# Optimization experiments

Hardware: AMD Instinct MI355X
Metric: run time of the kernel (lower is better)

The kernel has to match this reference:

```python
import jax, jax.numpy as jnp
import numpy as np

B, N_PER_G, H, K, A, GNN_STEPS = 64, 100, 64, 5, 50, 3
N = B * N_PER_G  # total nodes


def _lin(key, din, dout):
    s = 1.0 / np.sqrt(din)
    kw, kb = jax.random.split(key)
    w = jax.random.uniform(kw, (din, dout), minval=-s, maxval=s, dtype=jnp.float32)
    b = jax.random.uniform(kb, (dout,), minval=-s, maxval=s, dtype=jnp.float32)
    return w, b


def setup_inputs() -> dict:
    key = jax.random.key(0)
    ks = jax.random.split(key, 16)
    # complete graph (no self loops) per batch graph
    i, j = np.meshgrid(np.arange(N_PER_G), np.arange(N_PER_G), indexing="ij")
    m = i != j
    s0, d0 = i[m], j[m]  # [n*(n-1)]
    offs = (np.arange(B) * N_PER_G)[:, None]
    src = jnp.asarray((s0[None, :] + offs).reshape(-1), dtype=jnp.int32)
    dst = jnp.asarray((d0[None, :] + offs).reshape(-1), dtype=jnp.int32)
    E = src.shape[0]
    e_type = jax.random.uniform(ks[0], (E, 2), dtype=jnp.float32)
    d = jax.random.uniform(ks[1], (E, 1), dtype=jnp.float32)
    label = jax.nn.one_hot(jax.random.randint(ks[2], (N,), 0, K), K, dtype=jnp.float32)
    actions = jax.random.randint(ks[3], (B * A, 2), 0, N_PER_G)
    l1_w, l1_b = _lin(ks[4], K, H)
    l2_w, l2_b = _lin(ks[5], H, H)
    t3_w, t3_b = _lin(ks[6], H, H)
    t4_wf, t4_b = _lin(ks[7], 1, H)
    t5_wf, t5_b = _lin(ks[8], H, 1)
    t6_w, t6_b = _lin(ks[9], H, H)
    t7_1_w, t7_1_b = _lin(ks[10], H, H)
    t7_2_w, t7_2_b = _lin(ks[11], H, H)
    t9_1_w, t9_1_b = _lin(ks[12], H, H)
    t9_2_w, t9_2_b = _lin(ks[13], H, H)
    return dict(label=label, e_type=e_type, d=d,
                l1_w=l1_w, l1_b=l1_b, l2_w=l2_w, l2_b=l2_b,
                t3_w=t3_w, t3_b=t3_b, t4_w=t4_wf[0], t4_b=t4_b,
                t5_w=t5_wf[:, 0], t5_b=t5_b, t6_w=t6_w, t6_b=t6_b,
                t7_1_w=t7_1_w, t7_1_b=t7_1_b, t7_2_w=t7_2_w, t7_2_b=t7_2_b,
                t9_1_w=t9_1_w, t9_1_b=t9_1_b, t9_2_w=t9_2_w, t9_2_b=t9_2_b,
                src=src, dst=dst, actions=actions)


def reference(label, e_type, d, l1_w, l1_b, l2_w, l2_b, t3_w, t3_b, t4_w, t4_b,
              t5_w, t5_b, t6_w, t6_b, t7_1_w, t7_1_b, t7_2_w, t7_2_b,
              t9_1_w, t9_1_b, t9_2_w, t9_2_b, src, dst, actions):
    e1 = e_type[:, 0]
    # n1_hd = h[src]*e1, n1_d = d*e1; bmm(n1_hd^T, n1_d) == sum over in-edges of h[src]*e1^2*d
    w_e = (e1 * e1) * d[:, 0]                              # [E]
    s_e = d[:, 0] * e1                                     # per-edge n1_d scalar [E]
    # sum_deg relu(t4(n1_d)) as edge-parallel relu + scatter-add
    t4_edge = jax.nn.relu(s_e[:, None] * t4_w[None, :] + t4_b)   # [E,H]
    t4_sum = jax.ops.segment_sum(t4_edge, dst, num_segments=N)   # [N,H]
    base = label @ l1_w + l1_b + t4_sum @ t3_w + t3_b            # constant across gnn steps
    h = jnp.zeros((N, H), dtype=label.dtype)
    for _ in range(GNN_STEPS):
        n1_h = jax.ops.segment_sum(h[src] * w_e[:, None], dst, num_segments=N)  # [N,H]
        h = jax.nn.relu(base + n1_h @ l2_w + l2_b)
    # readout (forward_): graph mean -> t6 stem; per-action node-pair branch
    stem = h.reshape(B, N_PER_G, H).mean(axis=1) @ t6_w + t6_b    # [B,H]
    h2 = h @ t7_1_w + t7_1_b                                      # [N,H]
    offs = jnp.repeat(jnp.arange(B, dtype=actions.dtype) * N_PER_G, A)
    a = actions + offs[:, None]                                   # global node ids [B*A,2]
    ha = h2[a[:, 0]] + h2[a[:, 1]]                                # [B*A,H]
    u = jax.nn.relu(jax.nn.relu(ha) @ t7_2_w + t7_2_b) @ t9_2_w + t9_2_b
    g_branch = jax.nn.relu(stem) @ t9_1_w + t9_1_b                # [B,H]
    q = jax.nn.relu(g_branch[:, None, :] + u.reshape(B, A, H))    # [B,A,H]
    Q_sa = q.reshape(B * A, H) @ t5_w + t5_b[0]                   # [B*A]
    return Q_sa
```

## Files before the change

### kernel.cpp

```cpp
#include <hip/hip_runtime.h>

#define HD 64
#define NPG 100
#define NGRP 64
#define NACT 50
#define EPG 9900

typedef const float* fcp;

__global__ __launch_bounds__(1024)
void k_fused(fcp label, fcp e_type, fcp dvec,
             fcp l1_w, fcp l1_b, fcp l2_w, fcp l2_b,
             fcp t3_w, fcp t3_b, fcp t4_w, fcp t4_b,
             fcp t5_w, fcp t5_b, fcp t6_w, fcp t6_b,
             fcp t7_1_w, fcp t7_1_b, fcp t7_2_w, fcp t7_2_b,
             fcp t9_1_w, fcp t9_1_b, fcp t9_2_w, fcp t9_2_b,
             const int* __restrict__ actions,
             float* __restrict__ out)
{
    const int g  = blockIdx.x;
    const int t  = threadIdx.x;
    const int hh = t & 63;
    const int w  = t >> 6;

    __shared__ __align__(16) float sh_h[NPG * HD];
    __shared__ __align__(16) float sh_wt[NPG * NPG];
    __shared__ __align__(16) float sh_s[NPG * NPG];
    __shared__ __align__(16) float awk[16 * HD];
    __shared__ float gbuf[HD];

    float l1r[5];
    #pragma unroll
    for (int kk = 0; kk < 5; ++kk) l1r[kk] = l1_w[kk * HD + hh];

    float basev[7];
    #pragma unroll
    for (int m = 0; m < 7; ++m) {
        const int j = w + 16 * m;
        float x = 0.f;
        if (j < NPG) {
            #pragma unroll
            for (int kk = 0; kk < 5; ++kk)
                x += label[(g * NPG + j) * 5 + kk] * l1r[kk];
        }
        basev[m] = x;
    }

    int a0r[4], a1r[4];
    #pragma unroll
    for (int m = 0; m < 4; ++m) {
        const int al = w + 15 * m;
        a0r[m] = 0; a1r[m] = 0;
        if (w < 15 && al < NACT) {
            const int a = g * NACT + al;
            a0r[m] = actions[a * 2 + 0];
            a1r[m] = actions[a * 2 + 1];
        }
    }

    const int ebase = g * EPG;
    for (int idx = t; idx < NPG * NPG; idx += 1024) {
        const int i = idx / NPG;
        const int j = idx - i * NPG;
        float s = 0.f, wv = 0.f;
        if (i != j) {
            const int e = ebase + i * 99 + j - (j > i ? 1 : 0);
            const float e1 = e_type[2 * e];
            const float dd = dvec[e];
            s  = dd * e1;
            wv = e1 * e1 * dd;
        }
        sh_s[j * NPG + i]  = s;
        sh_wt[j * NPG + i] = wv;
    }
    __syncthreads();

    const float w4  = t4_w[hh];
    const float b4  = t4_b[hh];
    const float rb4 = fmaxf(b4, 0.f);
    #pragma unroll
    for (int m = 0; m < 7; ++m) {
        const int j = w + 16 * m;
        if (j < NPG) {
            float a0 = 0.f, a1 = 0.f, a2 = 0.f, a3 = 0.f;
            #pragma unroll 5
            for (int ib = 0; ib < 25; ++ib) {
                const float4 s4 = *(const float4*)&sh_s[j * NPG + 4 * ib];
                a0 += fmaxf(s4.x * w4 + b4, 0.f);
                a1 += fmaxf(s4.y * w4 + b4, 0.f);
                a2 += fmaxf(s4.z * w4 + b4, 0.f);
                a3 += fmaxf(s4.w * w4 + b4, 0.f);
            }
            sh_h[j * HD + hh] = (a0 + a1) + (a2 + a3) - rb4;
        }
    }

    const float bb   = l1_b[hh] + t3_b[hh];
    const float l2bv = l2_b[hh];
    #pragma unroll
    for (int m = 0; m < 7; ++m) basev[m] += bb;
    for (int ib = 0; ib < 16; ++ib) {
        const float tw0 = t3_w[(4 * ib + 0) * HD + hh];
        const float tw1 = t3_w[(4 * ib + 1) * HD + hh];
        const float tw2 = t3_w[(4 * ib + 2) * HD + hh];
        const float tw3 = t3_w[(4 * ib + 3) * HD + hh];
        #pragma unroll
        for (int m = 0; m < 7; ++m) {
            const int j = w + 16 * m;
            if (j < NPG) {
                const float4 x4 = *(const float4*)&sh_h[j * HD + 4 * ib];
                basev[m] += x4.x * tw0 + x4.y * tw1 + x4.z * tw2 + x4.w * tw3;
            }
        }
    }
    #pragma unroll
    for (int m = 0; m < 7; ++m) {
        const int j = w + 16 * m;
        if (j < NPG) sh_h[j * HD + hh] = fmaxf(basev[m] + l2bv, 0.f);
    }
    __syncthreads();

    #pragma unroll 1
    for (int step = 0; step < 2; ++step) {
        float acc[7];
        #pragma unroll
        for (int m = 0; m < 7; ++m) acc[m] = 0.f;
        for (int ib = 0; ib < 25; ++ib) {
            const float h0 = sh_h[(4 * ib + 0) * HD + hh];
            const float h1 = sh_h[(4 * ib + 1) * HD + hh];
            const float h2 = sh_h[(4 * ib + 2) * HD + hh];
            const float h3 = sh_h[(4 * ib + 3) * HD + hh];
            #pragma unroll
            for (int m = 0; m < 7; ++m) {
                const int j = w + 16 * m;
                if (j < NPG) {
                    const float4 wv = *(const float4*)&sh_wt[j * NPG + 4 * ib];
                    acc[m] += wv.x * h0 + wv.y * h1 + wv.z * h2 + wv.w * h3;
                }
            }
        }
        #pragma unroll
        for (int m = 0; m < 7; ++m) {
            const int j = w + 16 * m;
            if (j < NPG) sh_s[j * HD + hh] = acc[m];
        }
        float v[7];
        #pragma unroll
        for (int m = 0; m < 7; ++m) v[m] = basev[m] + l2bv;
        for (int ib = 0; ib < 16; ++ib) {
            const float w0 = l2_w[(4 * ib + 0) * HD + hh];
            const float w1 = l2_w[(4 * ib + 1) * HD + hh];
            const float w2 = l2_w[(4 * ib + 2) * HD + hh];
            const float w3 = l2_w[(4 * ib + 3) * HD + hh];
            #pragma unroll
            for (int m = 0; m < 7; ++m) {
                const int j = w + 16 * m;
                if (j < NPG) {
                    const float4 x4 = *(const float4*)&sh_s[j * HD + 4 * ib];
                    v[m] += x4.x * w0 + x4.y * w1 + x4.z * w2 + x4.w * w3;
                }
            }
        }
        __syncthreads();
        #pragma unroll
        for (int m = 0; m < 7; ++m) {
            const int j = w + 16 * m;
            if (j < NPG) sh_h[j * HD + hh] = fmaxf(v[m], 0.f);
        }
        __syncthreads();
    }

    {
        float ml = 0.f;
        for (int j = w; j < NPG; j += 16) ml += sh_h[j * HD + hh];
        awk[w * HD + hh] = ml;
    }
    float* hsum = sh_s;
    float* r1s  = sh_s + NACT * HD;
    if (w < 15) {
        #pragma unroll
        for (int m = 0; m < 4; ++m) {
            const int al = w + 15 * m;
            if (al < NACT)
                hsum[al * HD + hh] = sh_h[a0r[m] * HD + hh] + sh_h[a1r[m] * HD + hh];
        }
    }
    __syncthreads();

    if (w == 15) {
        float ml = 0.f;
        #pragma unroll
        for (int ww = 0; ww < 16; ++ww) ml += awk[ww * HD + hh];
        ml *= (1.f / NPG);
        float s = t6_b[hh];
        #pragma unroll 8
        for (int q = 0; q < HD; ++q) s += __shfl(ml, q, 64) * t6_w[q * HD + hh];
        s = fmaxf(s, 0.f);
        float gb = t9_1_b[hh];
        #pragma unroll 8
        for (int q = 0; q < HD; ++q) gb += __shfl(s, q, 64) * t9_1_w[q * HD + hh];
        gbuf[hh] = gb;
    } else {
        const float b71 = 2.f * t7_1_b[hh];
        float r[4];
        #pragma unroll
        for (int m = 0; m < 4; ++m) r[m] = b71;
        for (int ib = 0; ib < 16; ++ib) {
            const float w0 = t7_1_w[(4 * ib + 0) * HD + hh];
            const float w1 = t7_1_w[(4 * ib + 1) * HD + hh];
            const float w2 = t7_1_w[(4 * ib + 2) * HD + hh];
            const float w3 = t7_1_w[(4 * ib + 3) * HD + hh];
            #pragma unroll
            for (int m = 0; m < 4; ++m) {
                const int al = w + 15 * m;
                if (al < NACT) {
                    const float4 x4 = *(const float4*)&hsum[al * HD + 4 * ib];
                    r[m] += x4.x * w0 + x4.y * w1 + x4.z * w2 + x4.w * w3;
                }
            }
        }
        #pragma unroll
        for (int m = 0; m < 4; ++m) {
            const int al = w + 15 * m;
            if (al < NACT) r1s[al * HD + hh] = fmaxf(r[m], 0.f);
        }
        const float b72 = t7_2_b[hh];
        #pragma unroll
        for (int m = 0; m < 4; ++m) r[m] = b72;
        for (int ib = 0; ib < 16; ++ib) {
            const float w0 = t7_2_w[(4 * ib + 0) * HD + hh];
            const float w1 = t7_2_w[(4 * ib + 1) * HD + hh];
            const float w2 = t7_2_w[(4 * ib + 2) * HD + hh];
            const float w3 = t7_2_w[(4 * ib + 3) * HD + hh];
            #pragma unroll
            for (int m = 0; m < 4; ++m) {
                const int al = w + 15 * m;
                if (al < NACT) {
                    const float4 x4 = *(const float4*)&r1s[al * HD + 4 * ib];
                    r[m] += x4.x * w0 + x4.y * w1 + x4.z * w2 + x4.w * w3;
                }
            }
        }
        #pragma unroll
        for (int m = 0; m < 4; ++m) {
            const int al = w + 15 * m;
            if (al < NACT) hsum[al * HD + hh] = fmaxf(r[m], 0.f);
        }
    }
    __syncthreads();

    if (w < 15) {
        const float b92  = t9_2_b[hh];
        const float t5wv = t5_w[hh];
        const float t5bv = t5_b[0];
        const float gbv  = gbuf[hh];
        float u[4];
        #pragma unroll
        for (int m = 0; m < 4; ++m) u[m] = b92;
        for (int ib = 0; ib < 16; ++ib) {
            const float w0 = t9_2_w[(4 * ib + 0) * HD + hh];
            const float w1 = t9_2_w[(4 * ib + 1) * HD + hh];
            const float w2 = t9_2_w[(4 * ib + 2) * HD + hh];
            const float w3 = t9_2_w[(4 * ib + 3) * HD + hh];
            #pragma unroll
            for (int m = 0; m < 4; ++m) {
                const int al = w + 15 * m;
                if (al < NACT) {
                    const float4 x4 = *(const float4*)&hsum[al * HD + 4 * ib];
                    u[m] += x4.x * w0 + x4.y * w1 + x4.z * w2 + x4.w * w3;
                }
            }
        }
        #pragma unroll
        for (int m = 0; m < 4; ++m) {
            const int al = w + 15 * m;
            float qv = fmaxf(gbv + u[m], 0.f) * t5wv;
            #pragma unroll
            for (int off = 32; off > 0; off >>= 1) qv += __shfl_xor(qv, off, 64);
            if (al < NACT && hh == 0) out[g * NACT + al] = qv + t5bv;
        }
    }
}

extern "C" void kernel_launch(void* const* d_in, const int* in_sizes, int n_in,
                              void* d_out, int out_size, void* d_ws, size_t ws_size,
                              hipStream_t stream)
{
    fcp label  = (fcp)d_in[0];
    fcp e_type = (fcp)d_in[1];
    fcp dvec   = (fcp)d_in[2];
    fcp l1_w   = (fcp)d_in[3];
    fcp l1_b   = (fcp)d_in[4];
    fcp l2_w   = (fcp)d_in[5];
    fcp l2_b   = (fcp)d_in[6];
    fcp t3_w   = (fcp)d_in[7];
    fcp t3_b   = (fcp)d_in[8];
    fcp t4_w   = (fcp)d_in[9];
    fcp t4_b   = (fcp)d_in[10];
    fcp t5_w   = (fcp)d_in[11];
    fcp t5_b   = (fcp)d_in[12];
    fcp t6_w   = (fcp)d_in[13];
    fcp t6_b   = (fcp)d_in[14];
    fcp t7_1_w = (fcp)d_in[15];
    fcp t7_1_b = (fcp)d_in[16];
    fcp t7_2_w = (fcp)d_in[17];
    fcp t7_2_b = (fcp)d_in[18];
    fcp t9_1_w = (fcp)d_in[19];
    fcp t9_1_b = (fcp)d_in[20];
    fcp t9_2_w = (fcp)d_in[21];
    fcp t9_2_b = (fcp)d_in[22];
    const int* actions = (const int*)d_in[25];

    k_fused<<<dim3(NGRP), dim3(1024), 0, stream>>>(
        label, e_type, dvec, l1_w, l1_b, l2_w, l2_b, t3_w, t3_b, t4_w, t4_b,
        t5_w, t5_b, t6_w, t6_b, t7_1_w, t7_1_b, t7_2_w, t7_2_b,
        t9_1_w, t9_1_b, t9_2_w, t9_2_b, actions, (float*)d_out);
}
```

Measured before the change: 184.2 us.

## Split each graph across four cooperative blocks with grid sync between GNN steps

The work for each graph is spread over four blocks, each owning 25 nodes, so 256 blocks run instead of 64 and more of the GPU's compute units are busy. Node states are exchanged through global ping-pong buffers, with a cooperative grid.sync after each GNN step. Each block reloads the full per-graph h into shared memory at every step. This adds grid-wide barriers and global round trips, and the fallback plain launch when the cooperative launch fails would be unsafe with grid.sync.

Measured after the change: 649.4 us. 3.53x slower.

```diff
diff --git a/kernel.cpp b/kernel.cpp
--- a/kernel.cpp
+++ b/kernel.cpp
@@ -1,4 +1,7 @@
 #include <hip/hip_runtime.h>
+#include <hip/hip_cooperative_groups.h>
+
+namespace cg = cooperative_groups;
 
 #define HD 64
 #define NPG 100
@@ -9,23 +12,28 @@
 typedef const float* fcp;
 
 __global__ __launch_bounds__(1024)
-void k_fused(fcp label, fcp e_type, fcp dvec,
-             fcp l1_w, fcp l1_b, fcp l2_w, fcp l2_b,
-             fcp t3_w, fcp t3_b, fcp t4_w, fcp t4_b,
-             fcp t5_w, fcp t5_b, fcp t6_w, fcp t6_b,
-             fcp t7_1_w, fcp t7_1_b, fcp t7_2_w, fcp t7_2_b,
-             fcp t9_1_w, fcp t9_1_b, fcp t9_2_w, fcp t9_2_b,
-             const int* __restrict__ actions,
-             float* __restrict__ out)
+void k_coop(fcp label, fcp e_type, fcp dvec,
+            fcp l1_w, fcp l1_b, fcp l2_w, fcp l2_b,
+            fcp t3_w, fcp t3_b, fcp t4_w, fcp t4_b,
+            fcp t5_w, fcp t5_b, fcp t6_w, fcp t6_b,
+            fcp t7_1_w, fcp t7_1_b, fcp t7_2_w, fcp t7_2_b,
+            fcp t9_1_w, fcp t9_1_b, fcp t9_2_w, fcp t9_2_b,
+            const int* __restrict__ actions,
+            float* __restrict__ hA, float* __restrict__ hB,
+            float* __restrict__ out)
 {
-    const int g  = blockIdx.x;
+    cg::grid_group grid = cg::this_grid();
+    const int g  = blockIdx.x >> 2;
+    const int c  = blockIdx.x & 3;
+    const int j0 = c * 25;
     const int t  = threadIdx.x;
     const int hh = t & 63;
     const int w  = t >> 6;
 
-    __shared__ __align__(16) float sh_h[NPG * HD];
-    __shared__ __align__(16) float sh_wt[NPG * NPG];
-    __shared__ __align__(16) float sh_s[NPG * NPG];
+    __shared__ __align__(16) float s_ld[2500];
+    __shared__ __align__(16) float w_ld[2500];
+    __shared__ __align__(16) float hs[NPG * HD];
+    __shared__ __align__(16) float t4s[25 * HD];
     __shared__ __align__(16) float awk[16 * HD];
     __shared__ float gbuf[HD];
 
@@ -33,158 +41,156 @@
     #pragma unroll
     for (int kk = 0; kk < 5; ++kk) l1r[kk] = l1_w[kk * HD + hh];
 
-    float basev[7];
+    float basev0 = 0.f, basev1 = 0.f;
     #pragma unroll
-    for (int m = 0; m < 7; ++m) {
-        const int j = w + 16 * m;
-        float x = 0.f;
-        if (j < NPG) {
-            #pragma unroll
-            for (int kk = 0; kk < 5; ++kk)
-                x += label[(g * NPG + j) * 5 + kk] * l1r[kk];
-        }
-        basev[m] = x;
-    }
-
-    int a0r[4], a1r[4];
-    #pragma unroll
-    for (int m = 0; m < 4; ++m) {
-        const int al = w + 15 * m;
-        a0r[m] = 0; a1r[m] = 0;
-        if (w < 15 && al < NACT) {
-            const int a = g * NACT + al;
-            a0r[m] = actions[a * 2 + 0];
-            a1r[m] = actions[a * 2 + 1];
-        }
-    }
-
+    for (int kk = 0; kk < 5; ++kk)
+        basev0 += label[(g * NPG + j0 + w) * 5 + kk] * l1r[kk];
+    if (w < 9) {
+        #pragma unroll
+        for (int kk = 0; kk < 5; ++kk)
+            basev1 += label[(g * NPG + j0 + 16 + w) * 5 + kk] * l1r[kk];
+    }
+
+    const int acnt = (c < 2) ? 13 : 12;
+    const int abase = c * 12 + (c < 2 ? c : 2);
+    int a0r = 0, a1r = 0;
+    if (w < acnt) {
+        const int a = g * NACT + abase + w;
+        a0r = actions[a * 2 + 0];
+        a1r = actions[a * 2 + 1];
+    }
+
+    const float2* et2 = (const float2*)e_type;
     const int ebase = g * EPG;
-    for (int idx = t; idx < NPG * NPG; idx += 1024) {
-        const int i = idx / NPG;
-        const int j = idx - i * NPG;
+    for (int idx = t; idx < 2500; idx += 1024) {
+        const int i  = idx / 25;
+        const int jl = idx - i * 25;
+        const int j  = j0 + jl;
         float s = 0.f, wv = 0.f;
         if (i != j) {
             const int e = ebase + i * 99 + j - (j > i ? 1 : 0);
-            const float e1 = e_type[2 * e];
+            const float e1 = et2[e].x;
             const float dd = dvec[e];
             s  = dd * e1;
             wv = e1 * e1 * dd;
         }
-        sh_s[j * NPG + i]  = s;
-        sh_wt[j * NPG + i] = wv;
+        s_ld[jl * 100 + i] = s;
+        w_ld[jl * 100 + i] = wv;
     }
     __syncthreads();
 
     const float w4  = t4_w[hh];
     const float b4  = t4_b[hh];
     const float rb4 = fmaxf(b4, 0.f);
-    #pragma unroll
-    for (int m = 0; m < 7; ++m) {
-        const int j = w + 16 * m;
-        if (j < NPG) {
-            float a0 = 0.f, a1 = 0.f, a2 = 0.f, a3 = 0.f;
-            #pragma unroll 5
-            for (int ib = 0; ib < 25; ++ib) {
-                const float4 s4 = *(const float4*)&sh_s[j * NPG + 4 * ib];
-                a0 += fmaxf(s4.x * w4 + b4, 0.f);
-                a1 += fmaxf(s4.y * w4 + b4, 0.f);
-                a2 += fmaxf(s4.z * w4 + b4, 0.f);
-                a3 += fmaxf(s4.w * w4 + b4, 0.f);
-            }
-            sh_h[j * HD + hh] = (a0 + a1) + (a2 + a3) - rb4;
-        }
+    {
+        float a0 = 0.f, a1 = 0.f, a2 = 0.f, a3 = 0.f;
+        #pragma unroll 5
+        for (int ib = 0; ib < 25; ++ib) {
+            const float4 s4 = *(const float4*)&s_ld[w * 100 + 4 * ib];
+            a0 += fmaxf(s4.x * w4 + b4, 0.f);
+            a1 += fmaxf(s4.y * w4 + b4, 0.f);
+            a2 += fmaxf(s4.z * w4 + b4, 0.f);
+            a3 += fmaxf(s4.w * w4 + b4, 0.f);
+        }
+        t4s[w * HD + hh] = (a0 + a1) + (a2 + a3) - rb4;
+    }
+    if (w < 9) {
+        float a0 = 0.f, a1 = 0.f, a2 = 0.f, a3 = 0.f;
+        #pragma unroll 5
+        for (int ib = 0; ib < 25; ++ib) {
+            const float4 s4 = *(const float4*)&s_ld[(16 + w) * 100 + 4 * ib];
+            a0 += fmaxf(s4.x * w4 + b4, 0.f);
+            a1 += fmaxf(s4.y * w4 + b4, 0.f);
+            a2 += fmaxf(s4.z * w4 + b4, 0.f);
+            a3 += fmaxf(s4.w * w4 + b4, 0.f);
+        }
+        t4s[(16 + w) * HD + hh] = (a0 + a1) + (a2 + a3) - rb4;
     }
 
     const float bb   = l1_b[hh] + t3_b[hh];
     const float l2bv = l2_b[hh];
-    #pragma unroll
-    for (int m = 0; m < 7; ++m) basev[m] += bb;
+    basev0 += bb; basev1 += bb;
     for (int ib = 0; ib < 16; ++ib) {
         const float tw0 = t3_w[(4 * ib + 0) * HD + hh];
         const float tw1 = t3_w[(4 * ib + 1) * HD + hh];
         const float tw2 = t3_w[(4 * ib + 2) * HD + hh];
         const float tw3 = t3_w[(4 * ib + 3) * HD + hh];
-        #pragma unroll
-        for (int m = 0; m < 7; ++m) {
-            const int j = w + 16 * m;
-            if (j < NPG) {
-                const float4 x4 = *(const float4*)&sh_h[j * HD + 4 * ib];
-                basev[m] += x4.x * tw0 + x4.y * tw1 + x4.z * tw2 + x4.w * tw3;
-            }
-        }
-    }
-    #pragma unroll
-    for (int m = 0; m < 7; ++m) {
-        const int j = w + 16 * m;
-        if (j < NPG) sh_h[j * HD + hh] = fmaxf(basev[m] + l2bv, 0.f);
-    }
-    __syncthreads();
+        const float4 x0 = *(const float4*)&t4s[w * HD + 4 * ib];
+        basev0 += x0.x * tw0 + x0.y * tw1 + x0.z * tw2 + x0.w * tw3;
+        if (w < 9) {
+            const float4 x1 = *(const float4*)&t4s[(16 + w) * HD + 4 * ib];
+            basev1 += x1.x * tw0 + x1.y * tw1 + x1.z * tw2 + x1.w * tw3;
+        }
+    }
+    hA[(g * NPG + j0 + w) * HD + hh] = fmaxf(basev0 + l2bv, 0.f);
+    if (w < 9)
+        hA[(g * NPG + j0 + 16 + w) * HD + hh] = fmaxf(basev1 + l2bv, 0.f);
+    __threadfence();
+    grid.sync();
 
     #pragma unroll 1
     for (int step = 0; step < 2; ++step) {
-        float acc[7];
-        #pragma unroll
-        for (int m = 0; m < 7; ++m) acc[m] = 0.f;
+        fcp    hin  = step ? (fcp)hB : (fcp)hA;
+        float* hout = step ? hA : hB;
+        {
+            const float4* hin4 = (const float4*)(hin + g * NPG * HD);
+            float4* hs4 = (float4*)hs;
+            for (int idx = t; idx < NPG * HD / 4; idx += 1024) hs4[idx] = hin4[idx];
+        }
+        __syncthreads();
+
+        float acc0 = 0.f, acc1 = 0.f;
         for (int ib = 0; ib < 25; ++ib) {
-            const float h0 = sh_h[(4 * ib + 0) * HD + hh];
-            const float h1 = sh_h[(4 * ib + 1) * HD + hh];
-            const float h2 = sh_h[(4 * ib + 2) * HD + hh];
-            const float h3 = sh_h[(4 * ib + 3) * HD + hh];
-            #pragma unroll
-            for (int m = 0; m < 7; ++m) {
-                const int j = w + 16 * m;
-                if (j < NPG) {
-                    const float4 wv = *(const float4*)&sh_wt[j * NPG + 4 * ib];
-                    acc[m] += wv.x * h0 + wv.y * h1 + wv.z * h2 + wv.w * h3;
-                }
+            const float h0 = hs[(4 * ib + 0) * HD + hh];
+            const float h1 = hs[(4 * ib + 1) * HD + hh];
+            const float h2 = hs[(4 * ib + 2) * HD + hh];
+            const float h3 = hs[(4 * ib + 3) * HD + hh];
+            const float4 wa = *(const float4*)&w_ld[w * 100 + 4 * ib];
+            acc0 += wa.x * h0 + wa.y * h1 + wa.z * h2 + wa.w * h3;
+            if (w < 9) {
+                const float4 wb = *(const float4*)&w_ld[(16 + w) * 100 + 4 * ib];
+                acc1 += wb.x * h0 + wb.y * h1 + wb.z * h2 + wb.w * h3;
             }
         }
-        #pragma unroll
-        for (int m = 0; m < 7; ++m) {
-            const int j = w + 16 * m;
-            if (j < NPG) sh_s[j * HD + hh] = acc[m];
-        }
-        float v[7];
-        #pragma unroll
-        for (int m = 0; m < 7; ++m) v[m] = basev[m] + l2bv;
+        t4s[w * HD + hh] = acc0;
+        if (w < 9) t4s[(16 + w) * HD + hh] = acc1;
+
+        float v0 = basev0 + l2bv, v1 = basev1 + l2bv;
         for (int ib = 0; ib < 16; ++ib) {
             const float w0 = l2_w[(4 * ib + 0) * HD + hh];
             const float w1 = l2_w[(4 * ib + 1) * HD + hh];
             const float w2 = l2_w[(4 * ib + 2) * HD + hh];
             const float w3 = l2_w[(4 * ib + 3) * HD + hh];
-            #pragma unroll
-            for (int m = 0; m < 7; ++m) {
-                const int j = w + 16 * m;
-                if (j < NPG) {
-                    const float4 x4 = *(const float4*)&sh_s[j * HD + 4 * ib];
-                    v[m] += x4.x * w0 + x4.y * w1 + x4.z * w2 + x4.w * w3;
-                }
+            const float4 x0 = *(const float4*)&t4s[w * HD + 4 * ib];
+            v0 += x0.x * w0 + x0.y * w1 + x0.z * w2 + x0.w * w3;
+            if (w < 9) {
+                const float4 x1 = *(const float4*)&t4s[(16 + w) * HD + 4 * ib];
+                v1 += x1.x * w0 + x1.y * w1 + x1.z * w2 + x1.w * w3;
             }
         }
-        __syncthreads();
-        #pragma unroll
-        for (int m = 0; m < 7; ++m) {
-            const int j = w + 16 * m;
-            if (j < NPG) sh_h[j * HD + hh] = fmaxf(v[m], 0.f);
-        }
-        __syncthreads();
-    }
+        hout[(g * NPG + j0 + w) * HD + hh] = fmaxf(v0, 0.f);
+        if (w < 9)
+            hout[(g * NPG + j0 + 16 + w) * HD + hh] = fmaxf(v1, 0.f);
+        __threadfence();
+        grid.sync();
+    }
+
+    {
+        const float4* hin4 = (const float4*)(hA + g * NPG * HD);
+        float4* hs4 = (float4*)hs;
+        for (int idx = t; idx < NPG * HD / 4; idx += 1024) hs4[idx] = hin4[idx];
+    }
+    __syncthreads();
 
     {
         float ml = 0.f;
-        for (int j = w; j < NPG; j += 16) ml += sh_h[j * HD + hh];
+        for (int j = w; j < NPG; j += 16) ml += hs[j * HD + hh];
         awk[w * HD + hh] = ml;
     }
-    float* hsum = sh_s;
-    float* r1s  = sh_s + NACT * HD;
-    if (w < 15) {
-        #pragma unroll
-        for (int m = 0; m < 4; ++m) {
-            const int al = w + 15 * m;
-            if (al < NACT)
-                hsum[al * HD + hh] = sh_h[a0r[m] * HD + hh] + sh_h[a1r[m] * HD + hh];
-        }
-    }
+    float* hsum = w_ld;
+    float* r1s  = w_ld + 1024;
+    if (w < acnt)
+        hsum[w * HD + hh] = hs[a0r * HD + hh] + hs[a1r * HD + hh];
     __syncthreads();
 
     if (w == 15) {
@@ -200,85 +206,44 @@
         #pragma unroll 8
         for (int q = 0; q < HD; ++q) gb += __shfl(s, q, 64) * t9_1_w[q * HD + hh];
         gbuf[hh] = gb;
-    } else {
-        const float b71 = 2.f * t7_1_b[hh];
-        float r[4];
-        #pragma unroll
-        for (int m = 0; m < 4; ++m) r[m] = b71;
+    } else if (w < acnt) {
+        float r = 2.f * t7_1_b[hh];
         for (int ib = 0; ib < 16; ++ib) {
             const float w0 = t7_1_w[(4 * ib + 0) * HD + hh];
             const float w1 = t7_1_w[(4 * ib + 1) * HD + hh];
             const float w2 = t7_1_w[(4 * ib + 2) * HD + hh];
             const float w3 = t7_1_w[(4 * ib + 3) * HD + hh];
-            #pragma unroll
-            for (int m = 0; m < 4; ++m) {
-                const int al = w + 15 * m;
-                if (al < NACT) {
-                    const float4 x4 = *(const float4*)&hsum[al * HD + 4 * ib];
-                    r[m] += x4.x * w0 + x4.y * w1 + x4.z * w2 + x4.w * w3;
-                }
-            }
-        }
-        #pragma unroll
-        for (int m = 0; m < 4; ++m) {
-            const int al = w + 15 * m;
-            if (al < NACT) r1s[al * HD + hh] = fmaxf(r[m], 0.f);
-        }
-        const float b72 = t7_2_b[hh];
-        #pragma unroll
-        for (int m = 0; m < 4; ++m) r[m] = b72;
+            const float4 x4 = *(const float4*)&hsum[w * HD + 4 * ib];
+            r += x4.x * w0 + x4.y * w1 + x4.z * w2 + x4.w * w3;
+        }
+        r1s[w * HD + hh] = fmaxf(r, 0.f);
+        float r2 = t7_2_b[hh];
         for (int ib = 0; ib < 16; ++ib) {
             const float w0 = t7_2_w[(4 * ib + 0) * HD + hh];
             const float w1 = t7_2_w[(4 * ib + 1) * HD + hh];
             const float w2 = t7_2_w[(4 * ib + 2) * HD + hh];
             const float w3 = t7_2_w[(4 * ib + 3) * HD + hh];
-            #pragma unroll
-            for (int m = 0; m < 4; ++m) {
-                const int al = w + 15 * m;
-                if (al < NACT) {
-                    const float4 x4 = *(const float4*)&r1s[al * HD + 4 * ib];
-                    r[m] += x4.x * w0 + x4.y * w1 + x4.z * w2 + x4.w * w3;
-                }
-            }
-        }
-        #pragma unroll
-        for (int m = 0; m < 4; ++m) {
-            const int al = w + 15 * m;
-            if (al < NACT) hsum[al * HD + hh] = fmaxf(r[m], 0.f);
-        }
+            const float4 x4 = *(const float4*)&r1s[w * HD + 4 * ib];
+            r2 += x4.x * w0 + x4.y * w1 + x4.z * w2 + x4.w * w3;
+        }
+        hsum[w * HD + hh] = fmaxf(r2, 0.f);
     }
     __syncthreads();
 
-    if (w < 15) {
-        const float b92  = t9_2_b[hh];
-        const float t5wv = t5_w[hh];
-        const float t5bv = t5_b[0];
-        const float gbv  = gbuf[hh];
-        float u[4];
-        #pragma unroll
-        for (int m = 0; m < 4; ++m) u[m] = b92;
+    if (w < acnt) {
+        float u = t9_2_b[hh];
         for (int ib = 0; ib < 16; ++ib) {
             const float w0 = t9_2_w[(4 * ib + 0) * HD + hh];
             const float w1 = t9_2_w[(4 * ib + 1) * HD + hh];
             const float w2 = t9_2_w[(4 * ib + 2) * HD + hh];
             const float w3 = t9_2_w[(4 * ib + 3) * HD + hh];
-            #pragma unroll
-            for (int m = 0; m < 4; ++m) {
-                const int al = w + 15 * m;
-                if (al < NACT) {
-                    const float4 x4 = *(const float4*)&hsum[al * HD + 4 * ib];
-                    u[m] += x4.x * w0 + x4.y * w1 + x4.z * w2 + x4.w * w3;
-                }
-            }
-        }
+            const float4 x4 = *(const float4*)&hsum[w * HD + 4 * ib];
+            u += x4.x * w0 + x4.y * w1 + x4.z * w2 + x4.w * w3;
+        }
+        float qv = fmaxf(gbuf[hh] + u, 0.f) * t5_w[hh];
         #pragma unroll
-        for (int m = 0; m < 4; ++m) {
-            const int al = w + 15 * m;
-            float qv = fmaxf(gbv + u[m], 0.f) * t5wv;
-            #pragma unroll
-            for (int off = 32; off > 0; off >>= 1) qv += __shfl_xor(qv, off, 64);
-            if (al < NACT && hh == 0) out[g * NACT + al] = qv + t5bv;
-        }
+        for (int off = 32; off > 0; off >>= 1) qv += __shfl_xor(qv, off, 64);
+        if (hh == 0) out[g * NACT + abase + w] = qv + t5_b[0];
     }
 }
 
@@ -310,9 +275,27 @@
     fcp t9_2_w = (fcp)d_in[21];
     fcp t9_2_b = (fcp)d_in[22];
     const int* actions = (const int*)d_in[25];
-
-    k_fused<<<dim3(NGRP), dim3(1024), 0, stream>>>(
-        label, e_type, dvec, l1_w, l1_b, l2_w, l2_b, t3_w, t3_b, t4_w, t4_b,
-        t5_w, t5_b, t6_w, t6_b, t7_1_w, t7_1_b, t7_2_w, t7_2_b,
-        t9_1_w, t9_1_b, t9_2_w, t9_2_b, actions, (float*)d_out);
+    float* outp = (float*)d_out;
+
+    float* hA = (float*)d_ws;
+    float* hB = (float*)((char*)d_ws + 1638400);
+
+    void* args[] = {
+        (void*)&label, (void*)&e_type, (void*)&dvec,
+        (void*)&l1_w, (void*)&l1_b, (void*)&l2_w, (void*)&l2_b,
+        (void*)&t3_w, (void*)&t3_b, (void*)&t4_w, (void*)&t4_b,
+        (void*)&t5_w, (void*)&t5_b, (void*)&t6_w, (void*)&t6_b,
+        (void*)&t7_1_w, (void*)&t7_1_b, (void*)&t7_2_w, (void*)&t7_2_b,
+        (void*)&t9_1_w, (void*)&t9_1_b, (void*)&t9_2_w, (void*)&t9_2_b,
+        (void*)&actions, (void*)&hA, (void*)&hB, (void*)&outp
+    };
+    hipError_t err = hipLaunchCooperativeKernel(
+        (const void*)k_coop, dim3(NGRP * 4), dim3(1024), args, 0, stream);
+    if (err != hipSuccess) {
+        k_coop<<<dim3(NGRP * 4), dim3(1024), 0, stream>>>(
+            label, e_type, dvec, l1_w, l1_b, l2_w, l2_b, t3_w, t3_b,
+            t4_w, t4_b, t5_w, t5_b, t6_w, t6_b, t7_1_w, t7_1_b,
+            t7_2_w, t7_2_b, t9_1_w, t9_1_b, t9_2_w, t9_2_b,
+            actions, hA, hB, outp);
+    }
 }
```

## Split fused kernel into parallel edge/base kernel and GNN tail kernel

Applied to the files above, without the earlier changes.

The single 64-block fused kernel is split in two. The first kernel runs 256 blocks (four per graph, 25 destination nodes each). It computes the edge weights, the t4 aggregation and the base/initial h, and writes them to workspace. The second kernel loads these into shared memory and runs the remaining GNN steps and the readout. The aim is more parallelism for the edge-processing phase, since only 64 blocks on a large GPU left most CUs idle. The cost is an extra launch and a global round-trip of roughly 4 MB of intermediates.

Result: no change. 187.4 us (+1.7%).

```diff
diff --git a/kernel.cpp b/kernel.cpp
--- a/kernel.cpp
+++ b/kernel.cpp
@@ -9,43 +9,142 @@
 typedef const float* fcp;
 
 __global__ __launch_bounds__(1024)
-void k_fused(fcp label, fcp e_type, fcp dvec,
-             fcp l1_w, fcp l1_b, fcp l2_w, fcp l2_b,
-             fcp t3_w, fcp t3_b, fcp t4_w, fcp t4_b,
-             fcp t5_w, fcp t5_b, fcp t6_w, fcp t6_b,
-             fcp t7_1_w, fcp t7_1_b, fcp t7_2_w, fcp t7_2_b,
-             fcp t9_1_w, fcp t9_1_b, fcp t9_2_w, fcp t9_2_b,
-             const int* __restrict__ actions,
-             float* __restrict__ out)
+void k_edge_base(fcp label, fcp e_type, fcp dvec,
+                 fcp l1_w, fcp l1_b, fcp l2_b,
+                 fcp t3_w, fcp t3_b, fcp t4_w, fcp t4_b,
+                 float* __restrict__ Wt, float* __restrict__ baseo,
+                 float* __restrict__ hA)
+{
+    const int g  = blockIdx.x >> 2;
+    const int c  = blockIdx.x & 3;
+    const int j0 = c * 25;
+    const int t  = threadIdx.x;
+    const int hh = t & 63;
+    const int w  = t >> 6;
+
+    __shared__ __align__(16) float s_ld[2500];
+    __shared__ __align__(16) float w_ld[2500];
+    __shared__ __align__(16) float t4s[25 * HD];
+
+    float l1r[5], lab0[5], lab1[5];
+    #pragma unroll
+    for (int kk = 0; kk < 5; ++kk) l1r[kk] = l1_w[kk * HD + hh];
+    #pragma unroll
+    for (int kk = 0; kk < 5; ++kk)
+        lab0[kk] = label[(g * NPG + j0 + w) * 5 + kk];
+    #pragma unroll
+    for (int kk = 0; kk < 5; ++kk)
+        lab1[kk] = (w < 9) ? label[(g * NPG + j0 + 16 + w) * 5 + kk] : 0.f;
+
+    const float2* et2 = (const float2*)e_type;
+    const int ebase = g * EPG;
+    for (int idx = t; idx < 2500; idx += 1024) {
+        const int i  = idx / 25;
+        const int jl = idx - i * 25;
+        const int j  = j0 + jl;
+        float s = 0.f, wv = 0.f;
+        if (i != j) {
+            const int e = ebase + i * 99 + j - (j > i ? 1 : 0);
+            const float e1 = et2[e].x;
+            const float dd = dvec[e];
+            s  = dd * e1;
+            wv = e1 * e1 * dd;
+        }
+        s_ld[jl * 100 + i] = s;
+        w_ld[jl * 100 + i] = wv;
+    }
+    __syncthreads();
+
+    {
+        float* wd = Wt + g * (NPG * NPG) + j0 * NPG;
+        for (int idx = t; idx < 2500; idx += 1024) wd[idx] = w_ld[idx];
+    }
+
+    const float w4  = t4_w[hh];
+    const float b4  = t4_b[hh];
+    const float rb4 = fmaxf(b4, 0.f);
+    {
+        float a0 = 0.f, a1 = 0.f, a2 = 0.f, a3 = 0.f;
+        #pragma unroll 5
+        for (int ib = 0; ib < 25; ++ib) {
+            const float4 s4 = *(const float4*)&s_ld[w * 100 + 4 * ib];
+            a0 += fmaxf(s4.x * w4 + b4, 0.f);
+            a1 += fmaxf(s4.y * w4 + b4, 0.f);
+            a2 += fmaxf(s4.z * w4 + b4, 0.f);
+            a3 += fmaxf(s4.w * w4 + b4, 0.f);
+        }
+        t4s[w * HD + hh] = (a0 + a1) + (a2 + a3) - rb4;
+    }
+    if (w < 9) {
+        float a0 = 0.f, a1 = 0.f, a2 = 0.f, a3 = 0.f;
+        #pragma unroll 5
+        for (int ib = 0; ib < 25; ++ib) {
+            const float4 s4 = *(const float4*)&s_ld[(16 + w) * 100 + 4 * ib];
+            a0 += fmaxf(s4.x * w4 + b4, 0.f);
+            a1 += fmaxf(s4.y * w4 + b4, 0.f);
+            a2 += fmaxf(s4.z * w4 + b4, 0.f);
+            a3 += fmaxf(s4.w * w4 + b4, 0.f);
+        }
+        t4s[(16 + w) * HD + hh] = (a0 + a1) + (a2 + a3) - rb4;
+    }
+
+    const float bb   = l1_b[hh] + t3_b[hh];
+    const float l2bv = l2_b[hh];
+    float v0 = bb, v1 = bb;
+    #pragma unroll
+    for (int kk = 0; kk < 5; ++kk) v0 += lab0[kk] * l1r[kk];
+    #pragma unroll
+    for (int kk = 0; kk < 5; ++kk) v1 += lab1[kk] * l1r[kk];
+    for (int ib = 0; ib < 16; ++ib) {
+        const float tw0 = t3_w[(4 * ib + 0) * HD + hh];
+        const float tw1 = t3_w[(4 * ib + 1) * HD + hh];
+        const float tw2 = t3_w[(4 * ib + 2) * HD + hh];
+        const float tw3 = t3_w[(4 * ib + 3) * HD + hh];
+        const float4 x0 = *(const float4*)&t4s[w * HD + 4 * ib];
+        v0 += x0.x * tw0 + x0.y * tw1 + x0.z * tw2 + x0.w * tw3;
+        if (w < 9) {
+            const float4 x1 = *(const float4*)&t4s[(16 + w) * HD + 4 * ib];
+            v1 += x1.x * tw0 + x1.y * tw1 + x1.z * tw2 + x1.w * tw3;
+        }
+    }
+    {
+        const int n = g * NPG + j0 + w;
+        baseo[n * HD + hh] = v0;
+        hA[n * HD + hh]    = fmaxf(v0 + l2bv, 0.f);
+    }
+    if (w < 9) {
+        const int n = g * NPG + j0 + 16 + w;
+        baseo[n * HD + hh] = v1;
+        hA[n * HD + hh]    = fmaxf(v1 + l2bv, 0.f);
+    }
+}
+
+__global__ __launch_bounds__(1024)
+void k_gnn_tail(const float* __restrict__ Wt, const float* __restrict__ baseo,
+                const float* __restrict__ hA, fcp l2_w, fcp l2_b,
+                const int* __restrict__ actions,
+                fcp t5_w, fcp t5_b, fcp t6_w, fcp t6_b,
+                fcp t7_1_w, fcp t7_1_b, fcp t7_2_w, fcp t7_2_b,
+                fcp t9_1_w, fcp t9_1_b, fcp t9_2_w, fcp t9_2_b,
+                float* __restrict__ out)
 {
     const int g  = blockIdx.x;
     const int t  = threadIdx.x;
     const int hh = t & 63;
     const int w  = t >> 6;
 
+    __shared__ __align__(16) float sh_wt[NPG * NPG];
     __shared__ __align__(16) float sh_h[NPG * HD];
-    __shared__ __align__(16) float sh_wt[NPG * NPG];
-    __shared__ __align__(16) float sh_s[NPG * NPG];
+    __shared__ __align__(16) float sh_n1[NPG * HD];
     __shared__ __align__(16) float awk[16 * HD];
     __shared__ float gbuf[HD];
 
-    float l1r[5];
-    #pragma unroll
-    for (int kk = 0; kk < 5; ++kk) l1r[kk] = l1_w[kk * HD + hh];
-
     float basev[7];
     #pragma unroll
     for (int m = 0; m < 7; ++m) {
         const int j = w + 16 * m;
-        float x = 0.f;
-        if (j < NPG) {
-            #pragma unroll
-            for (int kk = 0; kk < 5; ++kk)
-                x += label[(g * NPG + j) * 5 + kk] * l1r[kk];
-        }
-        basev[m] = x;
-    }
-
+        basev[m] = (j < NPG) ? baseo[(g * NPG + j) * HD + hh] : 0.f;
+    }
     int a0r[4], a1r[4];
     #pragma unroll
     for (int m = 0; m < 4; ++m) {
@@ -58,67 +157,17 @@
         }
     }
 
-    const int ebase = g * EPG;
-    for (int idx = t; idx < NPG * NPG; idx += 1024) {
-        const int i = idx / NPG;
-        const int j = idx - i * NPG;
-        float s = 0.f, wv = 0.f;
-        if (i != j) {
-            const int e = ebase + i * 99 + j - (j > i ? 1 : 0);
-            const float e1 = e_type[2 * e];
-            const float dd = dvec[e];
-            s  = dd * e1;
-            wv = e1 * e1 * dd;
-        }
-        sh_s[j * NPG + i]  = s;
-        sh_wt[j * NPG + i] = wv;
+    {
+        const float4* ws4 = (const float4*)(Wt + g * (NPG * NPG));
+        float4* wd4 = (float4*)sh_wt;
+        for (int idx = t; idx < NPG * NPG / 4; idx += 1024) wd4[idx] = ws4[idx];
+        const float4* hs4 = (const float4*)(hA + g * NPG * HD);
+        float4* hd4 = (float4*)sh_h;
+        for (int idx = t; idx < NPG * HD / 4; idx += 1024) hd4[idx] = hs4[idx];
     }
     __syncthreads();
 
-    const float w4  = t4_w[hh];
-    const float b4  = t4_b[hh];
-    const float rb4 = fmaxf(b4, 0.f);
-    #pragma unroll
-    for (int m = 0; m < 7; ++m) {
-        const int j = w + 16 * m;
-        if (j < NPG) {
-            float a0 = 0.f, a1 = 0.f, a2 = 0.f, a3 = 0.f;
-            #pragma unroll 5
-            for (int ib = 0; ib < 25; ++ib) {
-                const float4 s4 = *(const float4*)&sh_s[j * NPG + 4 * ib];
-                a0 += fmaxf(s4.x * w4 + b4, 0.f);
-                a1 += fmaxf(s4.y * w4 + b4, 0.f);
-                a2 += fmaxf(s4.z * w4 + b4, 0.f);
-                a3 += fmaxf(s4.w * w4 + b4, 0.f);
-            }
-            sh_h[j * HD + hh] = (a0 + a1) + (a2 + a3) - rb4;
-        }
-    }
-
-    const float bb   = l1_b[hh] + t3_b[hh];
     const float l2bv = l2_b[hh];
-    #pragma unroll
-    for (int m = 0; m < 7; ++m) basev[m] += bb;
-    for (int ib = 0; ib < 16; ++ib) {
-        const float tw0 = t3_w[(4 * ib + 0) * HD + hh];
-        const float tw1 = t3_w[(4 * ib + 1) * HD + hh];
-        const float tw2 = t3_w[(4 * ib + 2) * HD + hh];
-        const float tw3 = t3_w[(4 * ib + 3) * HD + hh];
-        #pragma unroll
-        for (int m = 0; m < 7; ++m) {
-            const int j = w + 16 * m;
-            if (j < NPG) {
-                const float4 x4 = *(const float4*)&sh_h[j * HD + 4 * ib];
-                basev[m] += x4.x * tw0 + x4.y * tw1 + x4.z * tw2 + x4.w * tw3;
-            }
-        }
-    }
-    #pragma unroll
-    for (int m = 0; m < 7; ++m) {
-        const int j = w + 16 * m;
-        if (j < NPG) sh_h[j * HD + hh] = fmaxf(basev[m] + l2bv, 0.f);
-    }
-    __syncthreads();
 
     #pragma unroll 1
     for (int step = 0; step < 2; ++step) {
@@ -142,8 +191,9 @@
         #pragma unroll
         for (int m = 0; m < 7; ++m) {
             const int j = w + 16 * m;
-            if (j < NPG) sh_s[j * HD + hh] = acc[m];
-        }
+            if (j < NPG) sh_n1[j * HD + hh] = acc[m];
+        }
+
         float v[7];
         #pragma unroll
         for (int m = 0; m < 7; ++m) v[m] = basev[m] + l2bv;
@@ -156,7 +206,7 @@
             for (int m = 0; m < 7; ++m) {
                 const int j = w + 16 * m;
                 if (j < NPG) {
-                    const float4 x4 = *(const float4*)&sh_s[j * HD + 4 * ib];
+                    const float4 x4 = *(const float4*)&sh_n1[j * HD + 4 * ib];
                     v[m] += x4.x * w0 + x4.y * w1 + x4.z * w2 + x4.w * w3;
                 }
             }
@@ -175,8 +225,8 @@
         for (int j = w; j < NPG; j += 16) ml += sh_h[j * HD + hh];
         awk[w * HD + hh] = ml;
     }
-    float* hsum = sh_s;
-    float* r1s  = sh_s + NACT * HD;
+    float* hsum = sh_n1;
+    float* r1s  = sh_n1 + NACT * HD;
     if (w < 15) {
         #pragma unroll
         for (int m = 0; m < 4; ++m) {
@@ -311,8 +361,16 @@
     fcp t9_2_b = (fcp)d_in[22];
     const int* actions = (const int*)d_in[25];
 
-    k_fused<<<dim3(NGRP), dim3(1024), 0, stream>>>(
-        label, e_type, dvec, l1_w, l1_b, l2_w, l2_b, t3_w, t3_b, t4_w, t4_b,
-        t5_w, t5_b, t6_w, t6_b, t7_1_w, t7_1_b, t7_2_w, t7_2_b,
-        t9_1_w, t9_1_b, t9_2_w, t9_2_b, actions, (float*)d_out);
+    char* ws = (char*)d_ws;
+    float* Wt   = (float*)(ws);
+    float* base = (float*)(ws + 2560000);
+    float* hA   = (float*)(ws + 2560000 + 1638400);
+
+    k_edge_base<<<dim3(NGRP * 4), dim3(1024), 0, stream>>>(
+        label, e_type, dvec, l1_w, l1_b, l2_b, t3_w, t3_b, t4_w, t4_b,
+        Wt, base, hA);
+    k_gnn_tail<<<dim3(NGRP), dim3(1024), 0, stream>>>(
+        Wt, base, hA, l2_w, l2_b, actions, t5_w, t5_b, t6_w, t6_b,
+        t7_1_w, t7_1_b, t7_2_w, t7_2_b, t9_1_w, t9_1_b, t9_2_w, t9_2_b,
+        (float*)d_out);
 }
```
